# Performance work log

Measured on AMD Instinct MI355X. Metric: run time of the kernel, lower is better.

The kernel has to match this reference:

```python
import jax, jax.numpy as jnp
import numpy as np

DIM = 1024
NUM_HEADS = 16
HEAD_DIM = DIM // NUM_HEADS
B, L = 4, 4096


def setup_inputs() -> dict:
    key = jax.random.key(0)
    ks = jax.random.split(key, 11)
    s = 1.0 / np.sqrt(DIM)
    inp = {
        'q_seq': jax.random.normal(ks[0], (B, L, DIM), jnp.float32),
        'k_seq': jax.random.normal(ks[1], (B, L, DIM), jnp.float32),
        'v_seq': jax.random.normal(ks[2], (B, L, DIM), jnp.float32),
        'Wq': jax.random.normal(ks[3], (DIM, DIM), jnp.float32) * s,
        'bq': jax.random.normal(ks[4], (DIM,), jnp.float32) * s,
        'Wk': jax.random.normal(ks[5], (DIM, DIM), jnp.float32) * s,
        'bk': jax.random.normal(ks[6], (DIM,), jnp.float32) * s,
        'Wv': jax.random.normal(ks[7], (DIM, DIM), jnp.float32) * s,
        'bv': jax.random.normal(ks[8], (DIM,), jnp.float32) * s,
        'Wo': jax.random.normal(ks[9], (DIM, DIM), jnp.float32) * s,
        'bo': jax.random.normal(ks[10], (DIM,), jnp.float32) * s,
        'extract_common': 1,
    }
    return inp


def _heads(x):
    # [B, L, DIM] -> [B, H, L, D]
    Bb, Ll, _ = x.shape
    return x.reshape(Bb, Ll, NUM_HEADS, HEAD_DIM).transpose(0, 2, 1, 3)


def reference(q_seq, k_seq, v_seq, Wq, bq, Wk, bk, Wv, bv, Wo, bo, extract_common):
    Q = _heads(q_seq @ Wq.T + bq)   # [B, H, Lq, D]
    K = _heads(k_seq @ Wk.T + bk)   # [B, H, Lk, D]
    V = _heads(v_seq @ Wv.T + bv)   # [B, H, Lv, D]
    # softmax over the sequence dimension of K (torch dim=2 of [B,H,L,D])
    K_probs = jax.nn.softmax(K, axis=2)
    # context = K_probs^T @ V : [B, H, D, D]
    context = jnp.einsum('bhld,bhle->bhde', K_probs, V)
    attended = jnp.einsum('bhld,bhde->bhle', Q, context)  # [B, H, Lq, D]
    if extract_common:
        target = attended
    else:
        target = V - attended
    Bb, _, Ll, _ = target.shape
    target = target.transpose(0, 2, 1, 3).reshape(Bb, Ll, DIM)
    return target @ Wo.T + bo
```

## Files before the change

### kernel.cpp

```cpp
#include <hip/hip_runtime.h>
#include <cmath>

typedef __bf16 bf16x8 __attribute__((ext_vector_type(8)));
typedef float f32x4 __attribute__((ext_vector_type(4)));
typedef unsigned short us8 __attribute__((ext_vector_type(8)));

__device__ __forceinline__ unsigned short f2bf(float f) {
    union { float f; unsigned u; } x; x.f = f;
    unsigned u = x.u + 0x7FFFu + ((x.u >> 16) & 1u);
    return (unsigned short)(u >> 16);
}
__device__ __forceinline__ float bf2f(unsigned short h) {
    union { unsigned u; float f; } x; x.u = ((unsigned)h) << 16;
    return x.f;
}

__device__ __forceinline__ us8 cvt8(const float* p) {
    f32x4 a = *(const f32x4*)p;
    f32x4 b = *(const f32x4*)(p + 4);
    union { bf16x8 h; us8 u; } cv;
    cv.h[0] = (__bf16)a[0]; cv.h[1] = (__bf16)a[1];
    cv.h[2] = (__bf16)a[2]; cv.h[3] = (__bf16)a[3];
    cv.h[4] = (__bf16)b[0]; cv.h[5] = (__bf16)b[1];
    cv.h[6] = (__bf16)b[2]; cv.h[7] = (__bf16)b[3];
    return cv.u;
}

__device__ __forceinline__ void gl2lds16(const unsigned short* g, unsigned short* l) {
    __builtin_amdgcn_global_load_lds(
        (const __attribute__((address_space(1))) unsigned int*)g,
        (__attribute__((address_space(3))) unsigned int*)l, 16, 0, 0);
}

__global__ __launch_bounds__(256)
void cvt_kernel(const float* __restrict__ src, unsigned short* __restrict__ dst) {
    const size_t i = ((size_t)blockIdx.x * 256 + threadIdx.x) * 8;
    *(us8*)(dst + i) = cvt8(src + i);
}

template<int MODE, bool BF>
__global__ __launch_bounds__(256)
void gemm_proj(const void* __restrict__ Ap, const void* __restrict__ Wp,
               const float* __restrict__ bias,
               unsigned short* __restrict__ outT,
               float* __restrict__ S)
{
    __shared__ __align__(16) unsigned short lds[17408];
    unsigned short* ldsA = lds;
    unsigned short* ldsB = lds + 4096;

    const int tid = threadIdx.x;
    const int wid = tid >> 6, lane = tid & 63;
    const int quad = lane >> 4, l16 = lane & 15;
    const int waveM = wid >> 1, waveN = wid & 1;
    const int m0 = blockIdx.y * 128, n0 = blockIdx.x * 128;
    const int srow = tid >> 2;
    const int scol = (tid & 3) * 8;
    const int r4 = lane >> 2, c8 = (lane & 3) * 8;

    f32x4 acc[4][4] = {};

    for (int k0 = 0; k0 < 1024; k0 += 32) {
        __syncthreads();
        if (BF) {
            const unsigned short* A = (const unsigned short*)Ap;
            const unsigned short* W = (const unsigned short*)Wp;
            for (int s = wid; s < 8; s += 4) {
                const int row = s * 16 + r4;
                gl2lds16(A + (size_t)(m0 + row) * 1024 + k0 + c8, ldsA + s * 512);
                gl2lds16(W + (size_t)(n0 + row) * 1024 + k0 + c8, ldsB + s * 512);
            }
        } else {
            const float* A = (const float*)Ap;
            const float* W = (const float*)Wp;
#pragma unroll
            for (int p = 0; p < 2; ++p) {
                const int row = p * 64 + srow;
                *(us8*)(ldsA + row * 32 + scol) = cvt8(A + (size_t)(m0 + row) * 1024 + k0 + scol);
                *(us8*)(ldsB + row * 32 + scol) = cvt8(W + (size_t)(n0 + row) * 1024 + k0 + scol);
            }
        }
        __syncthreads();
        bf16x8 af[4], bfr[4];
#pragma unroll
        for (int i = 0; i < 4; ++i)
            af[i] = *(const bf16x8*)(ldsA + (waveM * 64 + i * 16 + l16) * 32 + quad * 8);
#pragma unroll
        for (int j = 0; j < 4; ++j)
            bfr[j] = *(const bf16x8*)(ldsB + (waveN * 64 + j * 16 + l16) * 32 + quad * 8);
#pragma unroll
        for (int i = 0; i < 4; ++i)
#pragma unroll
            for (int j = 0; j < 4; ++j)
                acc[i][j] = __builtin_amdgcn_mfma_f32_16x16x32_bf16(af[i], bfr[j], acc[i][j], 0, 0, 0);
    }

    __syncthreads();
    const int b = m0 >> 12, l0 = m0 & 4095;
#pragma unroll
    for (int j = 0; j < 4; ++j) {
        const int nn = waveN * 64 + j * 16 + l16;
        const float bc = bias[n0 + nn];
        float ssum = 0.f;
#pragma unroll
        for (int i = 0; i < 4; ++i)
#pragma unroll
            for (int r = 0; r < 4; ++r) {
                const int mm = waveM * 64 + i * 16 + quad * 4 + r;
                float v = acc[i][j][r] + bc;
                if (MODE == 1) v = expf(fminf(fmaxf(v, -30.f), 30.f));
                lds[nn * 136 + mm] = f2bf(v);
                ssum += v;
            }
        if (MODE == 1) {
            ssum += __shfl_xor(ssum, 16);
            ssum += __shfl_xor(ssum, 32);
            if (lane < 16)
                atomicAdd(&S[(size_t)b * 1024 + n0 + waveN * 64 + j * 16 + lane], ssum);
        }
    }
    __syncthreads();
    const int seg = (tid & 15) * 8;
#pragma unroll
    for (int it = 0; it < 8; ++it) {
        const int nn = (tid >> 4) + it * 16;
        us8 v = *(const us8*)&lds[nn * 136 + seg];
        *(us8*)(outT + ((size_t)b * 1024 + n0 + nn) * 4096 + l0 + seg) = v;
    }
}

__global__ __launch_bounds__(256)
void ctx_kernel(const unsigned short* __restrict__ Vt,
                const unsigned short* __restrict__ Et,
                float* __restrict__ ctxf)
{
    __shared__ __align__(16) unsigned short lds[4096];
    unsigned short* ldsA = lds;
    unsigned short* ldsB = lds + 2048;

    const int tid = threadIdx.x;
    const int wid = tid >> 6, lane = tid & 63;
    const int quad = lane >> 4, l16 = lane & 15;
    const int b = blockIdx.z, h = blockIdx.y;
    const int lbase = blockIdx.x * 1024;

    const unsigned short* Arow = Vt + ((size_t)b * 1024 + h * 64) * 4096;
    const unsigned short* Brow = Et + ((size_t)b * 1024 + h * 64) * 4096;

    const int srow = tid >> 2;
    const int scol = (tid & 3) * 8;

    f32x4 acc[4] = {};

    for (int k0 = 0; k0 < 1024; k0 += 32) {
        __syncthreads();
        us8 va = *(const us8*)(Arow + (size_t)srow * 4096 + lbase + k0 + scol);
        us8 vb = *(const us8*)(Brow + (size_t)srow * 4096 + lbase + k0 + scol);
        *(us8*)(ldsA + srow * 32 + scol) = va;
        *(us8*)(ldsB + srow * 32 + scol) = vb;
        __syncthreads();
        bf16x8 a = *(const bf16x8*)(ldsA + (wid * 16 + l16) * 32 + quad * 8);
#pragma unroll
        for (int j = 0; j < 4; ++j) {
            bf16x8 bb = *(const bf16x8*)(ldsB + (j * 16 + l16) * 32 + quad * 8);
            acc[j] = __builtin_amdgcn_mfma_f32_16x16x32_bf16(a, bb, acc[j], 0, 0, 0);
        }
    }
    float* base = ctxf + ((size_t)(b * 16 + h)) * 4096;
#pragma unroll
    for (int j = 0; j < 4; ++j)
#pragma unroll
        for (int r = 0; r < 4; ++r) {
            const int e = wid * 16 + quad * 4 + r;
            const int d = j * 16 + l16;
            atomicAdd(base + e * 64 + d, acc[j][r]);
        }
}

__global__ __launch_bounds__(256)
void ctx_norm(const float* __restrict__ ctxf, const float* __restrict__ S,
              unsigned short* __restrict__ ctxb)
{
    const int i = blockIdx.x * 256 + threadIdx.x;
    const int d = i & 63;
    const int bh = i >> 12;
    const int b = bh >> 4, h = bh & 15;
    ctxb[i] = f2bf(ctxf[i] / S[b * 1024 + h * 64 + d]);
}

template<bool BF>
__global__ __launch_bounds__(256)
void gemm_qattn(const void* __restrict__ Ap, const void* __restrict__ Wp,
                const float* __restrict__ bias,
                const unsigned short* __restrict__ ctxb,
                const unsigned short* __restrict__ Vt,
                const int* __restrict__ ec,
                unsigned short* __restrict__ att)
{
    __shared__ __align__(16) unsigned short lds[26624];
    unsigned short* ldsA = lds;
    unsigned short* ldsB = lds + 4096;
    unsigned short* ldsQ = lds;
    unsigned short* ldsC = lds + 17408;

    const int tid = threadIdx.x;
    const int wid = tid >> 6, lane = tid & 63;
    const int quad = lane >> 4, l16 = lane & 15;
    const int waveM = wid >> 1, waveN = wid & 1;
    const int m0 = blockIdx.y * 128, n0 = blockIdx.x * 128;
    const int b = m0 >> 12;
    const int srow = tid >> 2, scol = (tid & 3) * 8;
    const int r4 = lane >> 2, c8 = (lane & 3) * 8;

    {
        const int e2 = tid >> 1;
        const int sg = (tid & 1) * 32;
        const unsigned short* src = ctxb +
            (((size_t)(b * 16) + (n0 >> 6) + (e2 >> 6)) * 64 + (e2 & 63)) * 64 + sg;
#pragma unroll
        for (int u = 0; u < 4; ++u)
            *(us8*)&ldsC[e2 * 72 + sg + u * 8] = *(const us8*)(src + u * 8);
    }

    f32x4 acc[4][4] = {};

    for (int k0 = 0; k0 < 1024; k0 += 32) {
        __syncthreads();
        if (BF) {
            const unsigned short* A = (const unsigned short*)Ap;
            const unsigned short* W = (const unsigned short*)Wp;
            for (int s = wid; s < 8; s += 4) {
                const int row = s * 16 + r4;
                gl2lds16(A + (size_t)(m0 + row) * 1024 + k0 + c8, ldsA + s * 512);
                gl2lds16(W + (size_t)(n0 + row) * 1024 + k0 + c8, ldsB + s * 512);
            }
        } else {
            const float* A = (const float*)Ap;
            const float* W = (const float*)Wp;
#pragma unroll
            for (int p = 0; p < 2; ++p) {
                const int row = p * 64 + srow;
                *(us8*)(ldsA + row * 32 + scol) = cvt8(A + (size_t)(m0 + row) * 1024 + k0 + scol);
                *(us8*)(ldsB + row * 32 + scol) = cvt8(W + (size_t)(n0 + row) * 1024 + k0 + scol);
            }
        }
        __syncthreads();
        bf16x8 af[4], bfr[4];
#pragma unroll
        for (int i = 0; i < 4; ++i)
            af[i] = *(const bf16x8*)(ldsA + (waveM * 64 + i * 16 + l16) * 32 + quad * 8);
#pragma unroll
        for (int j = 0; j < 4; ++j)
            bfr[j] = *(const bf16x8*)(ldsB + (waveN * 64 + j * 16 + l16) * 32 + quad * 8);
#pragma unroll
        for (int i = 0; i < 4; ++i)
#pragma unroll
            for (int j = 0; j < 4; ++j)
                acc[i][j] = __builtin_amdgcn_mfma_f32_16x16x32_bf16(af[i], bfr[j], acc[i][j], 0, 0, 0);
    }

    __syncthreads();
#pragma unroll
    for (int j = 0; j < 4; ++j) {
        const int nn = waveN * 64 + j * 16 + l16;
        const float bc = bias[n0 + nn];
#pragma unroll
        for (int i = 0; i < 4; ++i)
#pragma unroll
            for (int r = 0; r < 4; ++r) {
                const int mm = waveM * 64 + i * 16 + quad * 4 + r;
                ldsQ[mm * 136 + nn] = f2bf(acc[i][j][r] + bc);
            }
    }
    __syncthreads();

    f32x4 acc2[4][4] = {};
#pragma unroll
    for (int ks = 0; ks < 64; ks += 32) {
        bf16x8 aq[4], cq[4];
#pragma unroll
        for (int i = 0; i < 4; ++i)
            aq[i] = *(const bf16x8*)&ldsQ[(waveM * 64 + i * 16 + l16) * 136 + waveN * 64 + ks + quad * 8];
#pragma unroll
        for (int j = 0; j < 4; ++j)
            cq[j] = *(const bf16x8*)&ldsC[(waveN * 64 + j * 16 + l16) * 72 + ks + quad * 8];
#pragma unroll
        for (int i = 0; i < 4; ++i)
#pragma unroll
            for (int j = 0; j < 4; ++j)
                acc2[i][j] = __builtin_amdgcn_mfma_f32_16x16x32_bf16(aq[i], cq[j], acc2[i][j], 0, 0, 0);
    }

    const int common = ec[0];
#pragma unroll
    for (int i = 0; i < 4; ++i)
#pragma unroll
        for (int j = 0; j < 4; ++j)
#pragma unroll
            for (int r = 0; r < 4; ++r) {
                const int lrow = m0 + waveM * 64 + i * 16 + quad * 4 + r;
                const int chan = n0 + waveN * 64 + j * 16 + l16;
                float vv = acc2[i][j][r];
                if (!common)
                    vv = bf2f(Vt[((size_t)(lrow >> 12) * 1024 + chan) * 4096 + (lrow & 4095)]) - vv;
                att[(size_t)lrow * 1024 + chan] = f2bf(vv);
            }
}

template<bool BF>
__global__ __launch_bounds__(256)
void gemm_out(const unsigned short* __restrict__ A, const void* __restrict__ Wp,
              const float* __restrict__ bias,
              float* __restrict__ outP)
{
    __shared__ __align__(16) unsigned short lds[8192];
    unsigned short* ldsA = lds;
    unsigned short* ldsB = lds + 4096;

    const int tid = threadIdx.x;
    const int wid = tid >> 6, lane = tid & 63;
    const int quad = lane >> 4, l16 = lane & 15;
    const int waveM = wid >> 1, waveN = wid & 1;
    const int m0 = blockIdx.y * 128, n0 = blockIdx.x * 128;
    const int srow = tid >> 2, scol = (tid & 3) * 8;
    const int r4 = lane >> 2, c8 = (lane & 3) * 8;

    f32x4 acc[4][4] = {};

    for (int k0 = 0; k0 < 1024; k0 += 32) {
        __syncthreads();
        if (BF) {
            const unsigned short* W = (const unsigned short*)Wp;
            for (int s = wid; s < 8; s += 4) {
                const int row = s * 16 + r4;
                gl2lds16(A + (size_t)(m0 + row) * 1024 + k0 + c8, ldsA + s * 512);
                gl2lds16(W + (size_t)(n0 + row) * 1024 + k0 + c8, ldsB + s * 512);
            }
        } else {
            const float* W = (const float*)Wp;
#pragma unroll
            for (int p = 0; p < 2; ++p) {
                const int row = p * 64 + srow;
                *(us8*)(ldsA + row * 32 + scol) = *(const us8*)(A + (size_t)(m0 + row) * 1024 + k0 + scol);
                *(us8*)(ldsB + row * 32 + scol) = cvt8(W + (size_t)(n0 + row) * 1024 + k0 + scol);
            }
        }
        __syncthreads();
        bf16x8 af[4], bfr[4];
#pragma unroll
        for (int i = 0; i < 4; ++i)
            af[i] = *(const bf16x8*)(ldsA + (waveM * 64 + i * 16 + l16) * 32 + quad * 8);
#pragma unroll
        for (int j = 0; j < 4; ++j)
            bfr[j] = *(const bf16x8*)(ldsB + (waveN * 64 + j * 16 + l16) * 32 + quad * 8);
#pragma unroll
        for (int i = 0; i < 4; ++i)
#pragma unroll
            for (int j = 0; j < 4; ++j)
                acc[i][j] = __builtin_amdgcn_mfma_f32_16x16x32_bf16(af[i], bfr[j], acc[i][j], 0, 0, 0);
    }

#pragma unroll
    for (int j = 0; j < 4; ++j) {
        const int col = n0 + waveN * 64 + j * 16 + l16;
        const float bc = bias[col];
#pragma unroll
        for (int i = 0; i < 4; ++i)
#pragma unroll
            for (int r = 0; r < 4; ++r) {
                const int row = m0 + waveM * 64 + i * 16 + quad * 4 + r;
                outP[(size_t)row * 1024 + col] = acc[i][j][r] + bc;
            }
    }
}

extern "C" void kernel_launch(void* const* d_in, const int* in_sizes, int n_in,
                              void* d_out, int out_size, void* d_ws, size_t ws_size,
                              hipStream_t stream)
{
    const float* q  = (const float*)d_in[0];
    const float* k  = (const float*)d_in[1];
    const float* v  = (const float*)d_in[2];
    const float* Wq = (const float*)d_in[3];
    const float* bq = (const float*)d_in[4];
    const float* Wk = (const float*)d_in[5];
    const float* bk = (const float*)d_in[6];
    const float* Wv = (const float*)d_in[7];
    const float* bv = (const float*)d_in[8];
    const float* Wo = (const float*)d_in[9];
    const float* bo = (const float*)d_in[10];
    const int* ec   = (const int*)d_in[11];

    char* ws = (char*)d_ws;
    const size_t NEED_FAST = 110641152;
    const dim3 gblk(8, 128, 1);

    if (ws_size >= NEED_FAST) {
        unsigned short* Ab   = (unsigned short*)(ws);
        unsigned short* Et   = (unsigned short*)(ws + 33554432);
        unsigned short* Vt   = (unsigned short*)(ws + 67108864);
        unsigned short* Wkb  = (unsigned short*)(ws + 100663296);
        unsigned short* Wvb  = (unsigned short*)(ws + 102760448);
        unsigned short* Wqb  = (unsigned short*)(ws + 104857600);
        unsigned short* Wob  = (unsigned short*)(ws + 106954752);
        float*          ctxf = (float*)(ws + 109051904);
        float*          S    = (float*)(ws + 110100480);
        unsigned short* ctxb = (unsigned short*)(ws + 110116864);
        unsigned short* att  = Et;

        hipMemsetAsync(S, 0, 4096 * sizeof(float), stream);
        hipMemsetAsync(ctxf, 0, 4 * 16 * 64 * 64 * sizeof(float), stream);

        cvt_kernel<<<512, 256, 0, stream>>>(Wk, Wkb);
        cvt_kernel<<<512, 256, 0, stream>>>(Wv, Wvb);
        cvt_kernel<<<512, 256, 0, stream>>>(Wq, Wqb);
        cvt_kernel<<<512, 256, 0, stream>>>(Wo, Wob);

        cvt_kernel<<<8192, 256, 0, stream>>>(k, Ab);
        gemm_proj<1, true><<<gblk, 256, 0, stream>>>(Ab, Wkb, bk, Et, S);

        cvt_kernel<<<8192, 256, 0, stream>>>(v, Ab);
        gemm_proj<2, true><<<gblk, 256, 0, stream>>>(Ab, Wvb, bv, Vt, nullptr);

        ctx_kernel<<<dim3(4, 16, 4), 256, 0, stream>>>(Vt, Et, ctxf);
        ctx_norm<<<1024, 256, 0, stream>>>(ctxf, S, ctxb);

        cvt_kernel<<<8192, 256, 0, stream>>>(q, Ab);
        gemm_qattn<true><<<gblk, 256, 0, stream>>>(Ab, Wqb, bq, ctxb, Vt, ec, att);

        gemm_out<true><<<gblk, 256, 0, stream>>>(att, Wob, bo, (float*)d_out);
    } else {
        unsigned short* Et   = (unsigned short*)(ws);
        unsigned short* Vt   = (unsigned short*)(ws + 33554432);
        float*          ctxf = (float*)(ws + 67108864);
        float*          S    = (float*)(ws + 68157440);
        unsigned short* ctxb = (unsigned short*)(ws + 68173824);
        unsigned short* att  = Et;

        hipMemsetAsync(S, 0, 4096 * sizeof(float), stream);
        hipMemsetAsync(ctxf, 0, 4 * 16 * 64 * 64 * sizeof(float), stream);

        gemm_proj<1, false><<<gblk, 256, 0, stream>>>(k, Wk, bk, Et, S);
        gemm_proj<2, false><<<gblk, 256, 0, stream>>>(v, Wv, bv, Vt, nullptr);
        ctx_kernel<<<dim3(4, 16, 4), 256, 0, stream>>>(Vt, Et, ctxf);
        ctx_norm<<<1024, 256, 0, stream>>>(ctxf, S, ctxb);
        gemm_qattn<false><<<gblk, 256, 0, stream>>>(q, Wq, bq, ctxb, Vt, ec, att);
        gemm_out<false><<<gblk, 256, 0, stream>>>(att, Wo, bo, (float*)d_out);
    }
}
```

Before: 510.4 us.

## Double-buffer GEMM LDS tiles, swizzle tile order, split ctx reduction, merge weight casts

Converts the projection, q-attention and output GEMMs to double-buffered LDS, issuing the load for the next K slice before the MFMAs on the current one, with one barrier per iteration instead of two. It also remaps block indices so consecutive blocks walk along M within a fixed N column, halves the ctx kernel's sequence chunk (doubling its grid) while register-prefetching its next slice, and folds the four weight-cast launches into one. The aim is to hide global-load latency behind the MFMAs and to cut launch count, at the cost of double the LDS per block and more atomic adds in the ctx reduction.

```diff
diff --git a/kernel.cpp b/kernel.cpp
--- a/kernel.cpp
+++ b/kernel.cpp
@@ -38,6 +38,26 @@
     *(us8*)(dst + i) = cvt8(src + i);
 }
 
+__global__ __launch_bounds__(256)
+void cvt_w4(const float* __restrict__ s0, const float* __restrict__ s1,
+            const float* __restrict__ s2, const float* __restrict__ s3,
+            unsigned short* __restrict__ d0, unsigned short* __restrict__ d1,
+            unsigned short* __restrict__ d2, unsigned short* __restrict__ d3) {
+    const float* sp[4] = {s0, s1, s2, s3};
+    unsigned short* dp[4] = {d0, d1, d2, d3};
+    const float* src = sp[blockIdx.y];
+    unsigned short* dst = dp[blockIdx.y];
+    const size_t i = ((size_t)blockIdx.x * 256 + threadIdx.x) * 8;
+    *(us8*)(dst + i) = cvt8(src + i);
+}
+
+__device__ __forceinline__ void swz_tiles(int& m0, int& n0) {
+    const int slot = blockIdx.x + (blockIdx.y << 3);
+    const int w = ((slot & 7) << 7) | (slot >> 3);
+    m0 = (w >> 3) << 7;
+    n0 = (w & 7) << 7;
+}
+
 template<int MODE, bool BF>
 __global__ __launch_bounds__(256)
 void gemm_proj(const void* __restrict__ Ap, const void* __restrict__ Wp,
@@ -46,41 +66,67 @@
                float* __restrict__ S)
 {
     __shared__ __align__(16) unsigned short lds[17408];
-    unsigned short* ldsA = lds;
-    unsigned short* ldsB = lds + 4096;
 
     const int tid = threadIdx.x;
     const int wid = tid >> 6, lane = tid & 63;
     const int quad = lane >> 4, l16 = lane & 15;
     const int waveM = wid >> 1, waveN = wid & 1;
-    const int m0 = blockIdx.y * 128, n0 = blockIdx.x * 128;
+    int m0, n0; swz_tiles(m0, n0);
     const int srow = tid >> 2;
     const int scol = (tid & 3) * 8;
     const int r4 = lane >> 2, c8 = (lane & 3) * 8;
 
     f32x4 acc[4][4] = {};
 
+    if (BF) {
+        const unsigned short* A = (const unsigned short*)Ap;
+        const unsigned short* W = (const unsigned short*)Wp;
+        for (int s = wid; s < 8; s += 4) {
+            const int row = s * 16 + r4;
+            gl2lds16(A + (size_t)(m0 + row) * 1024 + c8, lds + s * 512);
+            gl2lds16(W + (size_t)(n0 + row) * 1024 + c8, lds + 4096 + s * 512);
+        }
+    } else {
+        const float* A = (const float*)Ap;
+        const float* W = (const float*)Wp;
+#pragma unroll
+        for (int p = 0; p < 2; ++p) {
+            const int row = p * 64 + srow;
+            *(us8*)(lds + row * 32 + scol) = cvt8(A + (size_t)(m0 + row) * 1024 + scol);
+            *(us8*)(lds + 4096 + row * 32 + scol) = cvt8(W + (size_t)(n0 + row) * 1024 + scol);
+        }
+    }
+    __syncthreads();
+
+    int cur = 0;
     for (int k0 = 0; k0 < 1024; k0 += 32) {
-        __syncthreads();
-        if (BF) {
-            const unsigned short* A = (const unsigned short*)Ap;
-            const unsigned short* W = (const unsigned short*)Wp;
-            for (int s = wid; s < 8; s += 4) {
-                const int row = s * 16 + r4;
-                gl2lds16(A + (size_t)(m0 + row) * 1024 + k0 + c8, ldsA + s * 512);
-                gl2lds16(W + (size_t)(n0 + row) * 1024 + k0 + c8, ldsB + s * 512);
-            }
-        } else {
-            const float* A = (const float*)Ap;
-            const float* W = (const float*)Wp;
-#pragma unroll
-            for (int p = 0; p < 2; ++p) {
-                const int row = p * 64 + srow;
-                *(us8*)(ldsA + row * 32 + scol) = cvt8(A + (size_t)(m0 + row) * 1024 + k0 + scol);
-                *(us8*)(ldsB + row * 32 + scol) = cvt8(W + (size_t)(n0 + row) * 1024 + k0 + scol);
-            }
-        }
-        __syncthreads();
+        const int nxt = cur ^ 1;
+        if (k0 < 992) {
+            if (BF) {
+                const unsigned short* A = (const unsigned short*)Ap;
+                const unsigned short* W = (const unsigned short*)Wp;
+                for (int s = wid; s < 8; s += 4) {
+                    const int row = s * 16 + r4;
+                    gl2lds16(A + (size_t)(m0 + row) * 1024 + k0 + 32 + c8,
+                             lds + nxt * 8192 + s * 512);
+                    gl2lds16(W + (size_t)(n0 + row) * 1024 + k0 + 32 + c8,
+                             lds + nxt * 8192 + 4096 + s * 512);
+                }
+            } else {
+                const float* A = (const float*)Ap;
+                const float* W = (const float*)Wp;
+#pragma unroll
+                for (int p = 0; p < 2; ++p) {
+                    const int row = p * 64 + srow;
+                    *(us8*)(lds + nxt * 8192 + row * 32 + scol) =
+                        cvt8(A + (size_t)(m0 + row) * 1024 + k0 + 32 + scol);
+                    *(us8*)(lds + nxt * 8192 + 4096 + row * 32 + scol) =
+                        cvt8(W + (size_t)(n0 + row) * 1024 + k0 + 32 + scol);
+                }
+            }
+        }
+        const unsigned short* ldsA = lds + cur * 8192;
+        const unsigned short* ldsB = ldsA + 4096;
         bf16x8 af[4], bfr[4];
 #pragma unroll
         for (int i = 0; i < 4; ++i)
@@ -93,9 +139,10 @@
 #pragma unroll
             for (int j = 0; j < 4; ++j)
                 acc[i][j] = __builtin_amdgcn_mfma_f32_16x16x32_bf16(af[i], bfr[j], acc[i][j], 0, 0, 0);
-    }
-
-    __syncthreads();
+        __syncthreads();
+        cur = nxt;
+    }
+
     const int b = m0 >> 12, l0 = m0 & 4095;
 #pragma unroll
     for (int j = 0; j < 4; ++j) {
@@ -134,15 +181,13 @@
                 const unsigned short* __restrict__ Et,
                 float* __restrict__ ctxf)
 {
-    __shared__ __align__(16) unsigned short lds[4096];
-    unsigned short* ldsA = lds;
-    unsigned short* ldsB = lds + 2048;
+    __shared__ __align__(16) unsigned short lds[8192];
 
     const int tid = threadIdx.x;
     const int wid = tid >> 6, lane = tid & 63;
     const int quad = lane >> 4, l16 = lane & 15;
     const int b = blockIdx.z, h = blockIdx.y;
-    const int lbase = blockIdx.x * 1024;
+    const int lbase = blockIdx.x * 512;
 
     const unsigned short* Arow = Vt + ((size_t)b * 1024 + h * 64) * 4096;
     const unsigned short* Brow = Et + ((size_t)b * 1024 + h * 64) * 4096;
@@ -152,19 +197,37 @@
 
     f32x4 acc[4] = {};
 
-    for (int k0 = 0; k0 < 1024; k0 += 32) {
-        __syncthreads();
-        us8 va = *(const us8*)(Arow + (size_t)srow * 4096 + lbase + k0 + scol);
-        us8 vb = *(const us8*)(Brow + (size_t)srow * 4096 + lbase + k0 + scol);
-        *(us8*)(ldsA + srow * 32 + scol) = va;
-        *(us8*)(ldsB + srow * 32 + scol) = vb;
-        __syncthreads();
+    {
+        us8 va = *(const us8*)(Arow + (size_t)srow * 4096 + lbase + scol);
+        us8 vb = *(const us8*)(Brow + (size_t)srow * 4096 + lbase + scol);
+        *(us8*)(lds + srow * 32 + scol) = va;
+        *(us8*)(lds + 2048 + srow * 32 + scol) = vb;
+    }
+    __syncthreads();
+
+    int cur = 0;
+    for (int k0 = 0; k0 < 512; k0 += 32) {
+        const int nxt = cur ^ 1;
+        us8 na = {}, nb = {};
+        const bool pf = (k0 < 480);
+        if (pf) {
+            na = *(const us8*)(Arow + (size_t)srow * 4096 + lbase + k0 + 32 + scol);
+            nb = *(const us8*)(Brow + (size_t)srow * 4096 + lbase + k0 + 32 + scol);
+        }
+        const unsigned short* ldsA = lds + cur * 4096;
+        const unsigned short* ldsB = ldsA + 2048;
         bf16x8 a = *(const bf16x8*)(ldsA + (wid * 16 + l16) * 32 + quad * 8);
 #pragma unroll
         for (int j = 0; j < 4; ++j) {
             bf16x8 bb = *(const bf16x8*)(ldsB + (j * 16 + l16) * 32 + quad * 8);
             acc[j] = __builtin_amdgcn_mfma_f32_16x16x32_bf16(a, bb, acc[j], 0, 0, 0);
         }
+        if (pf) {
+            *(us8*)(lds + nxt * 4096 + srow * 32 + scol) = na;
+            *(us8*)(lds + nxt * 4096 + 2048 + srow * 32 + scol) = nb;
+        }
+        __syncthreads();
+        cur = nxt;
     }
     float* base = ctxf + ((size_t)(b * 16 + h)) * 4096;
 #pragma unroll
@@ -198,8 +261,6 @@
                 unsigned short* __restrict__ att)
 {
     __shared__ __align__(16) unsigned short lds[26624];
-    unsigned short* ldsA = lds;
-    unsigned short* ldsB = lds + 4096;
     unsigned short* ldsQ = lds;
     unsigned short* ldsC = lds + 17408;
 
@@ -207,7 +268,7 @@
     const int wid = tid >> 6, lane = tid & 63;
     const int quad = lane >> 4, l16 = lane & 15;
     const int waveM = wid >> 1, waveN = wid & 1;
-    const int m0 = blockIdx.y * 128, n0 = blockIdx.x * 128;
+    int m0, n0; swz_tiles(m0, n0);
     const int b = m0 >> 12;
     const int srow = tid >> 2, scol = (tid & 3) * 8;
     const int r4 = lane >> 2, c8 = (lane & 3) * 8;
@@ -224,27 +285,55 @@
 
     f32x4 acc[4][4] = {};
 
+    if (BF) {
+        const unsigned short* A = (const unsigned short*)Ap;
+        const unsigned short* W = (const unsigned short*)Wp;
+        for (int s = wid; s < 8; s += 4) {
+            const int row = s * 16 + r4;
+            gl2lds16(A + (size_t)(m0 + row) * 1024 + c8, lds + s * 512);
+            gl2lds16(W + (size_t)(n0 + row) * 1024 + c8, lds + 4096 + s * 512);
+        }
+    } else {
+        const float* A = (const float*)Ap;
+        const float* W = (const float*)Wp;
+#pragma unroll
+        for (int p = 0; p < 2; ++p) {
+            const int row = p * 64 + srow;
+            *(us8*)(lds + row * 32 + scol) = cvt8(A + (size_t)(m0 + row) * 1024 + scol);
+            *(us8*)(lds + 4096 + row * 32 + scol) = cvt8(W + (size_t)(n0 + row) * 1024 + scol);
+        }
+    }
+    __syncthreads();
+
+    int cur = 0;
     for (int k0 = 0; k0 < 1024; k0 += 32) {
-        __syncthreads();
-        if (BF) {
-            const unsigned short* A = (const unsigned short*)Ap;
-            const unsigned short* W = (const unsigned short*)Wp;
-            for (int s = wid; s < 8; s += 4) {
-                const int row = s * 16 + r4;
-                gl2lds16(A + (size_t)(m0 + row) * 1024 + k0 + c8, ldsA + s * 512);
-                gl2lds16(W + (size_t)(n0 + row) * 1024 + k0 + c8, ldsB + s * 512);
-            }
-        } else {
-            const float* A = (const float*)Ap;
-            const float* W = (const float*)Wp;
-#pragma unroll
-            for (int p = 0; p < 2; ++p) {
-                const int row = p * 64 + srow;
-                *(us8*)(ldsA + row * 32 + scol) = cvt8(A + (size_t)(m0 + row) * 1024 + k0 + scol);
-                *(us8*)(ldsB + row * 32 + scol) = cvt8(W + (size_t)(n0 + row) * 1024 + k0 + scol);
-            }
-        }
-        __syncthreads();
+        const int nxt = cur ^ 1;
+        if (k0 < 992) {
+            if (BF) {
+                const unsigned short* A = (const unsigned short*)Ap;
+                const unsigned short* W = (const unsigned short*)Wp;
+                for (int s = wid; s < 8; s += 4) {
+                    const int row = s * 16 + r4;
+                    gl2lds16(A + (size_t)(m0 + row) * 1024 + k0 + 32 + c8,
+                             lds + nxt * 8192 + s * 512);
+                    gl2lds16(W + (size_t)(n0 + row) * 1024 + k0 + 32 + c8,
+                             lds + nxt * 8192 + 4096 + s * 512);
+                }
+            } else {
+                const float* A = (const float*)Ap;
+                const float* W = (const float*)Wp;
+#pragma unroll
+                for (int p = 0; p < 2; ++p) {
+                    const int row = p * 64 + srow;
+                    *(us8*)(lds + nxt * 8192 + row * 32 + scol) =
+                        cvt8(A + (size_t)(m0 + row) * 1024 + k0 + 32 + scol);
+                    *(us8*)(lds + nxt * 8192 + 4096 + row * 32 + scol) =
+                        cvt8(W + (size_t)(n0 + row) * 1024 + k0 + 32 + scol);
+                }
+            }
+        }
+        const unsigned short* ldsA = lds + cur * 8192;
+        const unsigned short* ldsB = ldsA + 4096;
         bf16x8 af[4], bfr[4];
 #pragma unroll
         for (int i = 0; i < 4; ++i)
@@ -257,9 +346,10 @@
 #pragma unroll
             for (int j = 0; j < 4; ++j)
                 acc[i][j] = __builtin_amdgcn_mfma_f32_16x16x32_bf16(af[i], bfr[j], acc[i][j], 0, 0, 0);
-    }
-
-    __syncthreads();
+        __syncthreads();
+        cur = nxt;
+    }
+
 #pragma unroll
     for (int j = 0; j < 4; ++j) {
         const int nn = waveN * 64 + j * 16 + l16;
@@ -313,39 +403,63 @@
               const float* __restrict__ bias,
               float* __restrict__ outP)
 {
-    __shared__ __align__(16) unsigned short lds[8192];
-    unsigned short* ldsA = lds;
-    unsigned short* ldsB = lds + 4096;
+    __shared__ __align__(16) unsigned short lds[16384];
 
     const int tid = threadIdx.x;
     const int wid = tid >> 6, lane = tid & 63;
     const int quad = lane >> 4, l16 = lane & 15;
     const int waveM = wid >> 1, waveN = wid & 1;
-    const int m0 = blockIdx.y * 128, n0 = blockIdx.x * 128;
+    int m0, n0; swz_tiles(m0, n0);
     const int srow = tid >> 2, scol = (tid & 3) * 8;
     const int r4 = lane >> 2, c8 = (lane & 3) * 8;
 
     f32x4 acc[4][4] = {};
 
+    if (BF) {
+        const unsigned short* W = (const unsigned short*)Wp;
+        for (int s = wid; s < 8; s += 4) {
+            const int row = s * 16 + r4;
+            gl2lds16(A + (size_t)(m0 + row) * 1024 + c8, lds + s * 512);
+            gl2lds16(W + (size_t)(n0 + row) * 1024 + c8, lds + 4096 + s * 512);
+        }
+    } else {
+        const float* W = (const float*)Wp;
+#pragma unroll
+        for (int p = 0; p < 2; ++p) {
+            const int row = p * 64 + srow;
+            *(us8*)(lds + row * 32 + scol) = *(const us8*)(A + (size_t)(m0 + row) * 1024 + scol);
+            *(us8*)(lds + 4096 + row * 32 + scol) = cvt8(W + (size_t)(n0 + row) * 1024 + scol);
+        }
+    }
+    __syncthreads();
+
+    int cur = 0;
     for (int k0 = 0; k0 < 1024; k0 += 32) {
-        __syncthreads();
-        if (BF) {
-            const unsigned short* W = (const unsigned short*)Wp;
-            for (int s = wid; s < 8; s += 4) {
-                const int row = s * 16 + r4;
-                gl2lds16(A + (size_t)(m0 + row) * 1024 + k0 + c8, ldsA + s * 512);
-                gl2lds16(W + (size_t)(n0 + row) * 1024 + k0 + c8, ldsB + s * 512);
-            }
-        } else {
-            const float* W = (const float*)Wp;
-#pragma unroll
-            for (int p = 0; p < 2; ++p) {
-                const int row = p * 64 + srow;
-                *(us8*)(ldsA + row * 32 + scol) = *(const us8*)(A + (size_t)(m0 + row) * 1024 + k0 + scol);
-                *(us8*)(ldsB + row * 32 + scol) = cvt8(W + (size_t)(n0 + row) * 1024 + k0 + scol);
-            }
-        }
-        __syncthreads();
+        const int nxt = cur ^ 1;
+        if (k0 < 992) {
+            if (BF) {
+                const unsigned short* W = (const unsigned short*)Wp;
+                for (int s = wid; s < 8; s += 4) {
+                    const int row = s * 16 + r4;
+                    gl2lds16(A + (size_t)(m0 + row) * 1024 + k0 + 32 + c8,
+                             lds + nxt * 8192 + s * 512);
+                    gl2lds16(W + (size_t)(n0 + row) * 1024 + k0 + 32 + c8,
+                             lds + nxt * 8192 + 4096 + s * 512);
+                }
+            } else {
+                const float* W = (const float*)Wp;
+#pragma unroll
+                for (int p = 0; p < 2; ++p) {
+                    const int row = p * 64 + srow;
+                    *(us8*)(lds + nxt * 8192 + row * 32 + scol) =
+                        *(const us8*)(A + (size_t)(m0 + row) * 1024 + k0 + 32 + scol);
+                    *(us8*)(lds + nxt * 8192 + 4096 + row * 32 + scol) =
+                        cvt8(W + (size_t)(n0 + row) * 1024 + k0 + 32 + scol);
+                }
+            }
+        }
+        const unsigned short* ldsA = lds + cur * 8192;
+        const unsigned short* ldsB = ldsA + 4096;
         bf16x8 af[4], bfr[4];
 #pragma unroll
         for (int i = 0; i < 4; ++i)
@@ -358,6 +472,8 @@
 #pragma unroll
             for (int j = 0; j < 4; ++j)
                 acc[i][j] = __builtin_amdgcn_mfma_f32_16x16x32_bf16(af[i], bfr[j], acc[i][j], 0, 0, 0);
+        __syncthreads();
+        cur = nxt;
     }
 
 #pragma unroll
@@ -394,6 +510,7 @@
     char* ws = (char*)d_ws;
     const size_t NEED_FAST = 110641152;
     const dim3 gblk(8, 128, 1);
+    const dim3 gctx(8, 16, 4);
 
     if (ws_size >= NEED_FAST) {
         unsigned short* Ab   = (unsigned short*)(ws);
@@ -411,10 +528,7 @@
         hipMemsetAsync(S, 0, 4096 * sizeof(float), stream);
         hipMemsetAsync(ctxf, 0, 4 * 16 * 64 * 64 * sizeof(float), stream);
 
-        cvt_kernel<<<512, 256, 0, stream>>>(Wk, Wkb);
-        cvt_kernel<<<512, 256, 0, stream>>>(Wv, Wvb);
-        cvt_kernel<<<512, 256, 0, stream>>>(Wq, Wqb);
-        cvt_kernel<<<512, 256, 0, stream>>>(Wo, Wob);
+        cvt_w4<<<dim3(512, 4), 256, 0, stream>>>(Wk, Wv, Wq, Wo, Wkb, Wvb, Wqb, Wob);
 
         cvt_kernel<<<8192, 256, 0, stream>>>(k, Ab);
         gemm_proj<1, true><<<gblk, 256, 0, stream>>>(Ab, Wkb, bk, Et, S);
@@ -422,7 +536,7 @@
         cvt_kernel<<<8192, 256, 0, stream>>>(v, Ab);
         gemm_proj<2, true><<<gblk, 256, 0, stream>>>(Ab, Wvb, bv, Vt, nullptr);
 
-        ctx_kernel<<<dim3(4, 16, 4), 256, 0, stream>>>(Vt, Et, ctxf);
+        ctx_kernel<<<gctx, 256, 0, stream>>>(Vt, Et, ctxf);
         ctx_norm<<<1024, 256, 0, stream>>>(ctxf, S, ctxb);
 
         cvt_kernel<<<8192, 256, 0, stream>>>(q, Ab);
@@ -442,7 +556,7 @@
 
         gemm_proj<1, false><<<gblk, 256, 0, stream>>>(k, Wk, bk, Et, S);
         gemm_proj<2, false><<<gblk, 256, 0, stream>>>(v, Wv, bv, Vt, nullptr);
-        ctx_kernel<<<dim3(4, 16, 4), 256, 0, stream>>>(Vt, Et, ctxf);
+        ctx_kernel<<<gctx, 256, 0, stream>>>(Vt, Et, ctxf);
         ctx_norm<<<1024, 256, 0, stream>>>(ctxf, S, ctxb);
         gemm_qattn<false><<<gblk, 256, 0, stream>>>(q, Wq, bq, ctxb, Vt, ec, att);
         gemm_out<false><<<gblk, 256, 0, stream>>>(att, Wo, bo, (float*)d_out);
```

Result: faster. 458.3 us (-10.2%).
